# Kernel tuning notes

Measured on AMD Instinct MI355X. Metric: run time of the kernel, lower is better.

Reference implementation:

```python
import jax, jax.numpy as jnp
import numpy as np

B, L, D, H = 4, 2048, 1024, 16
HD = D // H

def setup_inputs() -> dict:
    key = jax.random.key(0)
    k1, k2, k3, k4 = jax.random.split(key, 4)
    return {
        "Q": jax.random.normal(k1, (B, L, D), dtype=jnp.float32),
        "K": jax.random.normal(k2, (B, L, D), dtype=jnp.float32),
        "V": jax.random.normal(k3, (B, L, D), dtype=jnp.float32),
        "W_out": jax.random.normal(k4, (D, D), dtype=jnp.float32) * (1.0 / np.sqrt(D)),
        "b_out": jnp.zeros((D,), dtype=jnp.float32),
    }

def reference(Q, K, V, W_out, b_out):
    b, l, d = Q.shape
    h, hd = H, d // H
    q = Q.reshape(b, l, h, hd)
    k = K.reshape(b, l, h, hd)
    v = V.reshape(b, l, h, hd)
    # energy: [b, h, q, k]
    energy = jnp.einsum('nqhd,nkhd->nhqk', q, k)
    # NOTE: original scales by sqrt(embed_dim), not sqrt(head_dim)
    attn = jax.nn.softmax(energy / jnp.sqrt(jnp.float32(d)), axis=-1)
    out = jnp.einsum('nhql,nlhd->nqhd', attn, v).reshape(b, l, d)
    # torch nn.Linear: x @ W.T + b
    return out @ W_out.T + b_out
```

## Files before the change

### kernel.cpp

```cpp
#include <hip/hip_runtime.h>
#include <hip/hip_bf16.h>


#define B_  4
#define L_  2048
#define D_  1024
#define H_  16

typedef float  f32x4  __attribute__((ext_vector_type(4)));
typedef short  bf16x8 __attribute__((ext_vector_type(8)));
typedef short  bf16x4 __attribute__((ext_vector_type(4)));

__device__ inline unsigned short f2bf(float x) {
    union { float f; unsigned u; } v; v.f = x;
    unsigned r = v.u + 0x7FFFu + ((v.u >> 16) & 1u);
    return (unsigned short)(r >> 16);
}
__device__ inline unsigned pack_trunc2(float lo, float hi) {
    union { float f; unsigned u; } a, b; a.f = lo; b.f = hi;
    return (a.u >> 16) | (b.u & 0xFFFF0000u);
}
__device__ inline float fast_exp2(float x) {
#if __has_builtin(__builtin_amdgcn_exp2f)
    return __builtin_amdgcn_exp2f(x);
#else
    return exp2f(x);
#endif
}
__device__ inline bf16x8 pack8s(float4 a, float4 b, float s) {
    bf16x8 r;
    r[0] = (short)f2bf(a.x * s); r[1] = (short)f2bf(a.y * s);
    r[2] = (short)f2bf(a.z * s); r[3] = (short)f2bf(a.w * s);
    r[4] = (short)f2bf(b.x * s); r[5] = (short)f2bf(b.y * s);
    r[6] = (short)f2bf(b.z * s); r[7] = (short)f2bf(b.w * s);
    return r;
}
__device__ inline void gld16(const void* g, void* l) {
    __builtin_amdgcn_global_load_lds(
        (const __attribute__((address_space(1))) void*)g,
        (__attribute__((address_space(3))) void*)l, 16, 0, 0);
}

__global__ __launch_bounds__(256) void convw_kernel(const float* __restrict__ W,
                                                    unsigned short* __restrict__ Wb) {
    int i = (blockIdx.x * 256 + threadIdx.x) * 4;
    float4 v = *(const float4*)&W[i];
    bf16x4 o;
    o[0] = (short)f2bf(v.x); o[1] = (short)f2bf(v.y);
    o[2] = (short)f2bf(v.z); o[3] = (short)f2bf(v.w);
    *(bf16x4*)&Wb[i] = o;
}

__global__ __launch_bounds__(256) void convk_kernel(const float* __restrict__ K,
                                                    unsigned short* __restrict__ Kb) {
    int o = blockIdx.x * 256 + threadIdx.x;
    int d8 = o & 7; int h = (o >> 3) & 15; int key = (o >> 7) & 2047; int b = o >> 18;
    size_t base = ((size_t)(b * L_ + key) * H_ + h) * 64;
    const float* p = K + base + d8 * 8;
    float4 a = *(const float4*)p, c = *(const float4*)(p + 4);
    bf16x8 r;
    r[0] = (short)f2bf(a.x); r[1] = (short)f2bf(a.y); r[2] = (short)f2bf(a.z); r[3] = (short)f2bf(a.w);
    r[4] = (short)f2bf(c.x); r[5] = (short)f2bf(c.y); r[6] = (short)f2bf(c.z); r[7] = (short)f2bf(c.w);
    *(bf16x8*)&Kb[base + ((d8 * 8) ^ ((key & 7) * 8))] = r;
}

__global__ __launch_bounds__(256) void convv_kernel(const float* __restrict__ V,
                                                    unsigned short* __restrict__ Vb) {
    __shared__ __align__(16) unsigned short T[64 * 72];
    int tid = threadIdx.x;
    int kb_ = blockIdx.x & 31, bh = blockIdx.x >> 5;
    int b = bh >> 4, h = bh & 15, k0 = kb_ * 64;
    int kl = tid >> 4;
    int d4 = (tid & 15) * 4;
    #pragma unroll
    for (int pp = 0; pp < 4; ++pp) {
        int key = pp * 16 + kl;
        const float* p = V + ((size_t)(b * L_ + k0 + key)) * D_ + h * 64 + d4;
        float4 v = *(const float4*)p;
        T[(d4 + 0) * 72 + key] = f2bf(v.x);
        T[(d4 + 1) * 72 + key] = f2bf(v.y);
        T[(d4 + 2) * 72 + key] = f2bf(v.z);
        T[(d4 + 3) * 72 + key] = f2bf(v.w);
    }
    __syncthreads();
    #pragma unroll
    for (int i = 0; i < 2; ++i) {
        int c = i * 256 + tid; int d = c >> 3, ch = c & 7;
        bf16x8 v = *(const bf16x8*)&T[d * 72 + ch * 8];
        *(bf16x8*)&Vb[((size_t)(b * H_ + h) * 64 + d) * L_ + k0 + ((ch ^ (d & 7)) * 8)] = v;
    }
}

__global__ __launch_bounds__(256, 4) void attn_kernel(const float* __restrict__ Qg,
                                                      const unsigned short* __restrict__ Kb,
                                                      const unsigned short* __restrict__ Vb,
                                                      unsigned short* __restrict__ Og) {
    __shared__ unsigned short Ks[2][64 * 64];
    __shared__ unsigned short Vt[2][64 * 64];

    const int tid  = threadIdx.x;
    const int w    = tid >> 6;
    const int lane = tid & 63;
    const int l16  = lane & 15;
    const int quad = lane >> 4;

    const int x   = blockIdx.x;
    const int idx = x >> 3;
    const int bh  = (x & 7) * 8 + (idx & 7);
    const int qb  = idx >> 3;
    const int bz  = bh >> 4;
    const int h   = bh & 15;
    const int q0  = qb * 128;

    const float qscale = 0.04508422f;
    bf16x8 aq[2][2];
    #pragma unroll
    for (int qt = 0; qt < 2; ++qt) {
        const int qrow = q0 + w * 32 + qt * 16 + l16;
        const float* qp = Qg + ((size_t)(bz * L_ + qrow)) * D_ + h * 64 + quad * 8;
        aq[qt][0] = pack8s(*(const float4*)qp,        *(const float4*)(qp + 4),  qscale);
        aq[qt][1] = pack8s(*(const float4*)(qp + 32), *(const float4*)(qp + 36), qscale);
    }

    f32x4 o[2][4];
    float lsum[2] = {0.f, 0.f};
    #pragma unroll
    for (int qt = 0; qt < 2; ++qt)
        #pragma unroll
        for (int i = 0; i < 4; ++i) o[qt][i] = (f32x4){0.f, 0.f, 0.f, 0.f};

    const unsigned short* Kbh = Kb + ((size_t)bz * L_ * H_ + h) * 64;
    const unsigned short* Vbh = Vb + (size_t)(bz * H_ + h) * 64 * L_;
    const int sw = (l16 & 7) * 8;
    const int hi = quad >> 1;
    const int i0 = (quad & 1) * 32 + l16;
    const int i1 = i0 + 16;

    #define ISSUE(T, BUF)                                                           \
        {                                                                           \
            int k0_ = (T) * 64;                                                     \
            _Pragma("unroll")                                                       \
            for (int i = 0; i < 2; ++i) {                                           \
                int c = i * 256 + tid; int rr = c >> 3, jj = c & 7;                 \
                gld16(Kbh + (size_t)(k0_ + rr) * (H_ * 64) + jj * 8,                \
                      (char*)Ks[BUF] + (i * 256 + w * 64) * 16);                    \
                gld16(Vbh + (size_t)rr * L_ + k0_ + jj * 8,                         \
                      (char*)Vt[BUF] + (i * 256 + w * 64) * 16);                    \
            }                                                                       \
        }

    ISSUE(0, 0)

    for (int t = 0; t < 32; ++t) {
        __syncthreads();
        if (t < 31) ISSUE(t + 1, (t + 1) & 1)
        const unsigned short* ks = Ks[t & 1];
        const unsigned short* vt = Vt[t & 1];

        f32x4 s[2][4];
        #pragma unroll
        for (int nt = 0; nt < 4; ++nt) {
            bf16x8 k0f = *(const bf16x8*)&ks[(nt * 16 + l16) * 64 + ((quad * 8) ^ sw)];
            bf16x8 k1f = *(const bf16x8*)&ks[(nt * 16 + l16) * 64 + ((32 + quad * 8) ^ sw)];
            #pragma unroll
            for (int qt = 0; qt < 2; ++qt) {
                f32x4 z = (f32x4){0.f, 0.f, 0.f, 0.f};
                z = __builtin_amdgcn_mfma_f32_16x16x32_bf16(k0f, aq[qt][0], z, 0, 0, 0);
                s[qt][nt] = __builtin_amdgcn_mfma_f32_16x16x32_bf16(k1f, aq[qt][1], z, 0, 0, 0);
            }
        }

        unsigned packed[2][4][2];
        #pragma unroll
        for (int qt = 0; qt < 2; ++qt)
            #pragma unroll
            for (int nt = 0; nt < 4; ++nt) {
                float p0 = fast_exp2(s[qt][nt][0]), p1 = fast_exp2(s[qt][nt][1]);
                float p2 = fast_exp2(s[qt][nt][2]), p3 = fast_exp2(s[qt][nt][3]);
                lsum[qt] += (p0 + p1) + (p2 + p3);
                packed[qt][nt][0] = pack_trunc2(p0, p1);
                packed[qt][nt][1] = pack_trunc2(p2, p3);
            }

        bf16x8 pav[2][2];
        #pragma unroll
        for (int qt = 0; qt < 2; ++qt) {
            union { int i[4]; bf16x8 v; } u0, u1;
            #pragma unroll
            for (int fp = 0; fp < 4; ++fp) {
                int src = (fp & 2) ? i1 : i0;
                int f   = fp & 1;
                int lo0 = __shfl((int)packed[qt][0][f], src);
                int hi0 = __shfl((int)packed[qt][1][f], src);
                u0.i[fp] = hi ? hi0 : lo0;
                int lo1 = __shfl((int)packed[qt][2][f], src);
                int hi1 = __shfl((int)packed[qt][3][f], src);
                u1.i[fp] = hi ? hi1 : lo1;
            }
            pav[qt][0] = u0.v; pav[qt][1] = u1.v;
        }

        #pragma unroll
        for (int dt = 0; dt < 4; ++dt) {
            bf16x8 v0 = *(const bf16x8*)&vt[(dt * 16 + l16) * 64 + ((quad * 8)      ^ sw)];
            bf16x8 v1 = *(const bf16x8*)&vt[(dt * 16 + l16) * 64 + ((32 + quad * 8) ^ sw)];
            #pragma unroll
            for (int qt = 0; qt < 2; ++qt) {
                o[qt][dt] = __builtin_amdgcn_mfma_f32_16x16x32_bf16(pav[qt][0], v0, o[qt][dt], 0, 0, 0);
                o[qt][dt] = __builtin_amdgcn_mfma_f32_16x16x32_bf16(pav[qt][1], v1, o[qt][dt], 0, 0, 0);
            }
        }
    }

    float tot[2];
    #pragma unroll
    for (int qt = 0; qt < 2; ++qt) {
        float v = lsum[qt];
        v += __shfl_xor(v, 16); v += __shfl_xor(v, 32);
        tot[qt] = v;
    }
    #pragma unroll
    for (int qt = 0; qt < 2; ++qt)
        #pragma unroll
        for (int r = 0; r < 4; ++r) {
            float tv  = __shfl(tot[qt], quad * 4 + r);
            float inv = 1.0f / tv;
            int q = q0 + w * 32 + qt * 16 + quad * 4 + r;
            size_t rowb = ((size_t)(bz * L_ + q)) * D_ + h * 64;
            #pragma unroll
            for (int dt = 0; dt < 4; ++dt)
                Og[rowb + dt * 16 + l16] = f2bf(o[qt][dt][r] * inv);
        }
}

__global__ __launch_bounds__(256, 2) void proj_kernel(const unsigned short* __restrict__ Og,
                                                      const unsigned short* __restrict__ Wb,
                                                      const float* __restrict__ bias,
                                                      float* __restrict__ Yg) {
    __shared__ unsigned short As[2][128 * 64];
    __shared__ unsigned short Bs[2][128 * 64];

    const int tid  = threadIdx.x;
    const int w    = tid >> 6;
    const int lane = tid & 63;
    const int l16  = lane & 15;
    const int quad = lane >> 4;
    const int wm   = w & 1, wn = w >> 1;

    const int m0 = blockIdx.x * 128;
    const int n0 = blockIdx.y * 128;

    f32x4 acc[4][4];
    #pragma unroll
    for (int i = 0; i < 4; ++i)
        #pragma unroll
        for (int j = 0; j < 4; ++j) acc[i][j] = (f32x4){0.f, 0.f, 0.f, 0.f};

    #define PISSUE(T, BUF)                                                          \
        {                                                                           \
            int kt_ = (T) * 64;                                                     \
            _Pragma("unroll")                                                       \
            for (int i = 0; i < 4; ++i) {                                           \
                int c = i * 256 + tid; int row = c >> 3, p = c & 7;                 \
                int j = p ^ (row & 7);                                              \
                gld16(&Og[(size_t)(m0 + row) * 1024 + kt_ + j * 8],                 \
                      (char*)As[BUF] + (i * 256 + w * 64) * 16);                    \
                gld16(&Wb[(size_t)(n0 + row) * 1024 + kt_ + j * 8],                 \
                      (char*)Bs[BUF] + (i * 256 + w * 64) * 16);                    \
            }                                                                       \
        }

    PISSUE(0, 0)

    for (int t = 0; t < 16; ++t) {
        __syncthreads();
        if (t < 15) PISSUE(t + 1, (t + 1) & 1)
        const unsigned short* as = As[t & 1];
        const unsigned short* bs = Bs[t & 1];

        #pragma unroll
        for (int ksq = 0; ksq < 2; ++ksq) {
            bf16x8 a[4], b[4];
            #pragma unroll
            for (int mt = 0; mt < 4; ++mt) {
                int row = wm * 64 + mt * 16 + l16;
                a[mt] = *(const bf16x8*)&as[row * 64 + (((ksq * 4 + quad) ^ (l16 & 7)) * 8)];
            }
            #pragma unroll
            for (int nt = 0; nt < 4; ++nt) {
                int row = wn * 64 + nt * 16 + l16;
                b[nt] = *(const bf16x8*)&bs[row * 64 + (((ksq * 4 + quad) ^ (l16 & 7)) * 8)];
            }
            #pragma unroll
            for (int mt = 0; mt < 4; ++mt)
                #pragma unroll
                for (int nt = 0; nt < 4; ++nt)
                    acc[mt][nt] = __builtin_amdgcn_mfma_f32_16x16x32_bf16(a[mt], b[nt], acc[mt][nt], 0, 0, 0);
        }
    }

    #pragma unroll
    for (int mt = 0; mt < 4; ++mt)
        #pragma unroll
        for (int nt = 0; nt < 4; ++nt) {
            int e = n0 + wn * 64 + nt * 16 + l16;
            float bv = bias[e];
            #pragma unroll
            for (int r = 0; r < 4; ++r) {
                int m = m0 + wm * 64 + mt * 16 + quad * 4 + r;
                Yg[(size_t)m * 1024 + e] = acc[mt][nt][r] + bv;
            }
        }
}

extern "C" void kernel_launch(void* const* d_in, const int* in_sizes, int n_in,
                              void* d_out, int out_size, void* d_ws, size_t ws_size,
                              hipStream_t stream) {
    const float* Q    = (const float*)d_in[0];
    const float* K    = (const float*)d_in[1];
    const float* V    = (const float*)d_in[2];
    const float* W    = (const float*)d_in[3];
    const float* bias = (const float*)d_in[4];
    float* Y = (float*)d_out;

    unsigned short* Og = (unsigned short*)d_ws;
    unsigned short* Wb = (unsigned short*)((char*)d_ws + (size_t)16 * 1024 * 1024);
    unsigned short* Kb = (unsigned short*)d_out;
    unsigned short* Vb = Kb + (size_t)B_ * H_ * L_ * 64;

    convw_kernel<<<D_ * D_ / (256 * 4), 256, 0, stream>>>(W, Wb);
    convk_kernel<<<B_ * L_ * H_ * 8 / 256, 256, 0, stream>>>(K, Kb);
    convv_kernel<<<B_ * H_ * (L_ / 64), 256, 0, stream>>>(V, Vb);
    attn_kernel<<<B_ * H_ * (L_ / 128), 256, 0, stream>>>(Q, Kb, Vb, Og);
    dim3 pg(B_ * L_ / 128, D_ / 128);
    proj_kernel<<<pg, 256, 0, stream>>>(Og, Wb, bias, Y);
}
```

Before: 256.7 us.

## Switch attention to 32x32x16 MFMA with permlane swap for P layout

Rewrites the attention inner loop to use 32x32x16 bf16 MFMA tiles instead of 16x16x32, so each wave computes a 32-query by 32-key score tile per instruction. The P matrix is converted with the hardware v_cvt_pk_bf16_f32 instruction and rearranged into the PV operand layout with v_permlane32_swap rather than many cross-lane shuffles. The intent is fewer MFMA issues, fewer LDS fragment loads and much less shuffle overhead. The trade-offs are larger accumulator register footprint, which may affect occupancy, and a changed output store pattern.

New measurement: 237.6 us. 7.5% less time.

```diff
diff --git a/kernel.cpp b/kernel.cpp
--- a/kernel.cpp
+++ b/kernel.cpp
@@ -8,6 +8,7 @@
 #define H_  16
 
 typedef float  f32x4  __attribute__((ext_vector_type(4)));
+typedef float  f32x16 __attribute__((ext_vector_type(16)));
 typedef short  bf16x8 __attribute__((ext_vector_type(8)));
 typedef short  bf16x4 __attribute__((ext_vector_type(4)));
 
@@ -15,10 +16,6 @@
     union { float f; unsigned u; } v; v.f = x;
     unsigned r = v.u + 0x7FFFu + ((v.u >> 16) & 1u);
     return (unsigned short)(r >> 16);
-}
-__device__ inline unsigned pack_trunc2(float lo, float hi) {
-    union { float f; unsigned u; } a, b; a.f = lo; b.f = hi;
-    return (a.u >> 16) | (b.u & 0xFFFF0000u);
 }
 __device__ inline float fast_exp2(float x) {
 #if __has_builtin(__builtin_amdgcn_exp2f)
@@ -34,6 +31,19 @@
     r[4] = (short)f2bf(b.x * s); r[5] = (short)f2bf(b.y * s);
     r[6] = (short)f2bf(b.z * s); r[7] = (short)f2bf(b.w * s);
     return r;
+}
+__device__ inline unsigned cvtpk(float lo, float hi) {
+    unsigned r;
+    asm("v_cvt_pk_bf16_f32 %0, %1, %2" : "=v"(r) : "v"(lo), "v"(hi));
+    return r;
+}
+#define PSWAP(a, b) asm("v_permlane32_swap_b32 %0, %1" : "+v"(a), "+v"(b))
+
+__device__ inline f32x16 zero16() {
+    f32x16 z;
+    #pragma unroll
+    for (int i = 0; i < 16; ++i) z[i] = 0.f;
+    return z;
 }
 __device__ inline void gld16(const void* g, void* l) {
     __builtin_amdgcn_global_load_lds(
@@ -95,14 +105,15 @@
                                                       const unsigned short* __restrict__ Kb,
                                                       const unsigned short* __restrict__ Vb,
                                                       unsigned short* __restrict__ Og) {
-    __shared__ unsigned short Ks[2][64 * 64];
-    __shared__ unsigned short Vt[2][64 * 64];
+    __shared__ __align__(16) unsigned short Ks[2][64 * 64];
+    __shared__ __align__(16) unsigned short Vt[2][64 * 64];
 
     const int tid  = threadIdx.x;
     const int w    = tid >> 6;
     const int lane = tid & 63;
-    const int l16  = lane & 15;
-    const int quad = lane >> 4;
+    const int l31  = lane & 31;
+    const int hl   = lane >> 5;
+    const int r7   = l31 & 7;
 
     const int x   = blockIdx.x;
     const int idx = x >> 3;
@@ -113,28 +124,22 @@
     const int q0  = qb * 128;
 
     const float qscale = 0.04508422f;
-    bf16x8 aq[2][2];
-    #pragma unroll
-    for (int qt = 0; qt < 2; ++qt) {
-        const int qrow = q0 + w * 32 + qt * 16 + l16;
-        const float* qp = Qg + ((size_t)(bz * L_ + qrow)) * D_ + h * 64 + quad * 8;
-        aq[qt][0] = pack8s(*(const float4*)qp,        *(const float4*)(qp + 4),  qscale);
-        aq[qt][1] = pack8s(*(const float4*)(qp + 32), *(const float4*)(qp + 36), qscale);
-    }
-
-    f32x4 o[2][4];
-    float lsum[2] = {0.f, 0.f};
-    #pragma unroll
-    for (int qt = 0; qt < 2; ++qt)
-        #pragma unroll
-        for (int i = 0; i < 4; ++i) o[qt][i] = (f32x4){0.f, 0.f, 0.f, 0.f};
+    bf16x8 bq[4];
+    {
+        const int qrow = q0 + w * 32 + l31;
+        const float* qp = Qg + ((size_t)(bz * L_ + qrow)) * D_ + h * 64 + hl * 8;
+        #pragma unroll
+        for (int dstep = 0; dstep < 4; ++dstep)
+            bq[dstep] = pack8s(*(const float4*)(qp + dstep * 16),
+                               *(const float4*)(qp + dstep * 16 + 4), qscale);
+    }
+
+    f32x16 o[2];
+    o[0] = zero16(); o[1] = zero16();
+    float lsum = 0.f;
 
     const unsigned short* Kbh = Kb + ((size_t)bz * L_ * H_ + h) * 64;
     const unsigned short* Vbh = Vb + (size_t)(bz * H_ + h) * 64 * L_;
-    const int sw = (l16 & 7) * 8;
-    const int hi = quad >> 1;
-    const int i0 = (quad & 1) * 32 + l16;
-    const int i1 = i0 + 16;
 
     #define ISSUE(T, BUF)                                                           \
         {                                                                           \
@@ -157,80 +162,55 @@
         const unsigned short* ks = Ks[t & 1];
         const unsigned short* vt = Vt[t & 1];
 
-        f32x4 s[2][4];
-        #pragma unroll
-        for (int nt = 0; nt < 4; ++nt) {
-            bf16x8 k0f = *(const bf16x8*)&ks[(nt * 16 + l16) * 64 + ((quad * 8) ^ sw)];
-            bf16x8 k1f = *(const bf16x8*)&ks[(nt * 16 + l16) * 64 + ((32 + quad * 8) ^ sw)];
-            #pragma unroll
-            for (int qt = 0; qt < 2; ++qt) {
-                f32x4 z = (f32x4){0.f, 0.f, 0.f, 0.f};
-                z = __builtin_amdgcn_mfma_f32_16x16x32_bf16(k0f, aq[qt][0], z, 0, 0, 0);
-                s[qt][nt] = __builtin_amdgcn_mfma_f32_16x16x32_bf16(k1f, aq[qt][1], z, 0, 0, 0);
-            }
-        }
-
-        unsigned packed[2][4][2];
-        #pragma unroll
-        for (int qt = 0; qt < 2; ++qt)
-            #pragma unroll
-            for (int nt = 0; nt < 4; ++nt) {
-                float p0 = fast_exp2(s[qt][nt][0]), p1 = fast_exp2(s[qt][nt][1]);
-                float p2 = fast_exp2(s[qt][nt][2]), p3 = fast_exp2(s[qt][nt][3]);
-                lsum[qt] += (p0 + p1) + (p2 + p3);
-                packed[qt][nt][0] = pack_trunc2(p0, p1);
-                packed[qt][nt][1] = pack_trunc2(p2, p3);
-            }
-
-        bf16x8 pav[2][2];
-        #pragma unroll
-        for (int qt = 0; qt < 2; ++qt) {
-            union { int i[4]; bf16x8 v; } u0, u1;
-            #pragma unroll
-            for (int fp = 0; fp < 4; ++fp) {
-                int src = (fp & 2) ? i1 : i0;
-                int f   = fp & 1;
-                int lo0 = __shfl((int)packed[qt][0][f], src);
-                int hi0 = __shfl((int)packed[qt][1][f], src);
-                u0.i[fp] = hi ? hi0 : lo0;
-                int lo1 = __shfl((int)packed[qt][2][f], src);
-                int hi1 = __shfl((int)packed[qt][3][f], src);
-                u1.i[fp] = hi ? hi1 : lo1;
-            }
-            pav[qt][0] = u0.v; pav[qt][1] = u1.v;
-        }
-
-        #pragma unroll
-        for (int dt = 0; dt < 4; ++dt) {
-            bf16x8 v0 = *(const bf16x8*)&vt[(dt * 16 + l16) * 64 + ((quad * 8)      ^ sw)];
-            bf16x8 v1 = *(const bf16x8*)&vt[(dt * 16 + l16) * 64 + ((32 + quad * 8) ^ sw)];
-            #pragma unroll
-            for (int qt = 0; qt < 2; ++qt) {
-                o[qt][dt] = __builtin_amdgcn_mfma_f32_16x16x32_bf16(pav[qt][0], v0, o[qt][dt], 0, 0, 0);
-                o[qt][dt] = __builtin_amdgcn_mfma_f32_16x16x32_bf16(pav[qt][1], v1, o[qt][dt], 0, 0, 0);
-            }
-        }
-    }
-
-    float tot[2];
-    #pragma unroll
-    for (int qt = 0; qt < 2; ++qt) {
-        float v = lsum[qt];
-        v += __shfl_xor(v, 16); v += __shfl_xor(v, 32);
-        tot[qt] = v;
-    }
-    #pragma unroll
-    for (int qt = 0; qt < 2; ++qt)
-        #pragma unroll
-        for (int r = 0; r < 4; ++r) {
-            float tv  = __shfl(tot[qt], quad * 4 + r);
-            float inv = 1.0f / tv;
-            int q = q0 + w * 32 + qt * 16 + quad * 4 + r;
-            size_t rowb = ((size_t)(bz * L_ + q)) * D_ + h * 64;
-            #pragma unroll
-            for (int dt = 0; dt < 4; ++dt)
-                Og[rowb + dt * 16 + l16] = f2bf(o[qt][dt][r] * inv);
-        }
+        #pragma unroll
+        for (int kk = 0; kk < 2; ++kk) {
+            f32x16 s = zero16();
+            #pragma unroll
+            for (int dstep = 0; dstep < 4; ++dstep) {
+                bf16x8 kf = *(const bf16x8*)&ks[(kk * 32 + l31) * 64 +
+                                                ((((dstep << 1) | hl) ^ r7) << 3)];
+                s = __builtin_amdgcn_mfma_f32_32x32x16_bf16(kf, bq[dstep], s, 0, 0, 0);
+            }
+
+            float p_[16];
+            #pragma unroll
+            for (int r = 0; r < 16; ++r) p_[r] = fast_exp2(s[r]);
+            lsum += ((p_[0] + p_[1]) + (p_[2] + p_[3])) + ((p_[4] + p_[5]) + (p_[6] + p_[7]))
+                  + ((p_[8] + p_[9]) + (p_[10] + p_[11])) + ((p_[12] + p_[13]) + (p_[14] + p_[15]));
+            unsigned pk_[8];
+            #pragma unroll
+            for (int j = 0; j < 8; ++j) pk_[j] = cvtpk(p_[2 * j], p_[2 * j + 1]);
+            PSWAP(pk_[0], pk_[2]); PSWAP(pk_[1], pk_[3]);
+            PSWAP(pk_[4], pk_[6]); PSWAP(pk_[5], pk_[7]);
+            union { unsigned u[4]; bf16x8 v; } a0_, a1_;
+            a0_.u[0] = pk_[0]; a0_.u[1] = pk_[1]; a0_.u[2] = pk_[2]; a0_.u[3] = pk_[3];
+            a1_.u[0] = pk_[4]; a1_.u[1] = pk_[5]; a1_.u[2] = pk_[6]; a1_.u[3] = pk_[7];
+
+            #pragma unroll
+            for (int kh = 0; kh < 2; ++kh) {
+                const bf16x8 pf = kh ? a1_.v : a0_.v;
+                const int kk2 = kk * 2 + kh;
+                bf16x8 v0 = *(const bf16x8*)&vt[(l31) * 64 +
+                                                ((((kk2 << 1) | hl) ^ r7) << 3)];
+                bf16x8 v1 = *(const bf16x8*)&vt[(32 + l31) * 64 +
+                                                ((((kk2 << 1) | hl) ^ r7) << 3)];
+                o[0] = __builtin_amdgcn_mfma_f32_32x32x16_bf16(pf, v0, o[0], 0, 0, 0);
+                o[1] = __builtin_amdgcn_mfma_f32_32x32x16_bf16(pf, v1, o[1], 0, 0, 0);
+            }
+        }
+    }
+
+    float tot = lsum + __shfl_xor(lsum, 32);
+    float inv = 1.0f / tot;
+    const size_t rowb0 = ((size_t)(bz * L_ + q0 + w * 32)) * D_ + h * 64;
+    #pragma unroll
+    for (int r = 0; r < 16; ++r) {
+        const int qloc = (r & 3) + 8 * (r >> 2) + 4 * hl;
+        const float invr = __shfl(inv, qloc);
+        unsigned short* op = Og + rowb0 + (size_t)qloc * D_;
+        op[l31]      = f2bf(o[0][r] * invr);
+        op[32 + l31] = f2bf(o[1][r] * invr);
+    }
 }
 
 __global__ __launch_bounds__(256, 2) void proj_kernel(const unsigned short* __restrict__ Og,
```
